# Kernel optimization log

Measured on AMD Instinct MI355X. Metric: run time of the kernel, lower is better.

## Reference

```python
import jax, jax.numpy as jnp
import numpy as np


def _grid_sample_points(feat, gx, gy):
    """Bilinear grid_sample at point list, align_corners=False, zeros padding.
    feat: [B, H, W, C]; gx, gy: [B, N] normalized coords in [-1, 1].
    Returns [B, N, C].
    """
    B, H, W, C = feat.shape
    # unnormalize (align_corners=False): -1 -> -0.5, +1 -> size-0.5
    ix = (gx + 1.0) * (W * 0.5) - 0.5
    iy = (gy + 1.0) * (H * 0.5) - 0.5
    x0 = jnp.floor(ix)
    y0 = jnp.floor(iy)
    x1 = x0 + 1.0
    y1 = y0 + 1.0
    wx1 = ix - x0
    wx0 = 1.0 - wx1
    wy1 = iy - y0
    wy0 = 1.0 - wy1
    bidx = jnp.arange(B)[:, None]  # [B,1] broadcasts against [B,N]

    def gather(yy, xx):
        valid = (xx >= 0) & (xx <= W - 1) & (yy >= 0) & (yy <= H - 1)
        xi = jnp.clip(xx, 0, W - 1).astype(jnp.int32)
        yi = jnp.clip(yy, 0, H - 1).astype(jnp.int32)
        v = feat[bidx, yi, xi]  # [B, N, C]
        return v * valid[..., None].astype(feat.dtype)

    out = (gather(y0, x0) * (wy0 * wx0)[..., None]
           + gather(y0, x1) * (wy0 * wx1)[..., None]
           + gather(y1, x0) * (wy1 * wx0)[..., None]
           + gather(y1, x1) * (wy1 * wx1)[..., None])
    return out


def setup_inputs() -> dict:
    key = jax.random.key(0)
    k1, k2, k3, k4, k5 = jax.random.split(key, 5)
    B, C, T, Wd, Hd = 16, 64, 16, 36, 36
    N, D = 4096, C * T  # num_neurons, num_input
    x = jax.random.normal(k1, (B, C, T, Wd, Hd), dtype=jnp.float32)
    mu = jax.random.uniform(k2, (N, 2), minval=-1.0, maxval=1.0, dtype=jnp.float32)
    sigma = jax.random.uniform(k3, (N,), dtype=jnp.float32)  # unused in eval mode
    W = jax.random.normal(k4, (N, D), dtype=jnp.float32) * 0.02
    b = jax.random.normal(k5, (N,), dtype=jnp.float32) * 0.01
    return {"x": x, "mu": mu, "sigma": sigma, "W": W, "b": b}


def reference(x, mu, sigma, W, b):
    # eval-mode forward (self.training == False): grid = mu broadcast over batch
    B, C, T, Wd, Hd = x.shape
    N = mu.shape[0]
    # torch: x.view(B, C*T, Wd, Hd); grid_sample treats dim2 as H_in, dim3 as W_in
    feat = x.reshape(B, C * T, Wd, Hd).transpose(0, 2, 3, 1)
    g = jnp.clip(mu, -1.0, 1.0)
    gx = jnp.broadcast_to(g[:, 0], (B, N))  # grid[...,0] indexes W_in
    gy = jnp.broadcast_to(g[:, 1], (B, N))  # grid[...,1] indexes H_in
    sampled = _grid_sample_points(feat, gx, gy)  # [B, N, C*T]
    # PoissonLinearReadout 3D path == per-neuron dot product (diagonal of full matmul)
    y = jnp.einsum('bnc,nc->bn', sampled, W) + b
    return jax.nn.elu(y) + 1.0
```

## Files before the change

kernel.cpp:

```cpp
#include <hip/hip_runtime.h>
#include <hip/hip_bf16.h>
#include <cmath>

#define CT    1024
#define PIX   1296
#define BATCH 16
#define NNEUR 4096
#define HW    36
#define NBINS (HW * HW)
#define NPAIR (NNEUR * 4)
#define BCT   (BATCH * CT)

typedef short short8 __attribute__((ext_vector_type(8)));
typedef float f32x4  __attribute__((ext_vector_type(4)));

__device__ __forceinline__ unsigned short bfu(float f) {
    __hip_bfloat16 h = __float2bfloat16(f);
    return *reinterpret_cast<unsigned short*>(&h);
}

__global__ __launch_bounds__(256) void transpose_bf16_kernel(
    const float* __restrict__ x, __hip_bfloat16* __restrict__ feat)
{
    __shared__ unsigned short lds[64][34];
    const int b      = blockIdx.z;
    const int ctBase = blockIdx.y * 64;
    const int pBase  = blockIdx.x * 32;
    const int t      = threadIdx.x;
    const size_t xb  = (size_t)b * CT * PIX;
    {
        const int r  = t >> 2;
        const int pc = (t & 3) * 8;
        const float* src = x + xb + (size_t)(ctBase + r) * PIX + pBase + pc;
        if (pBase + 32 <= PIX) {
            float4 a = reinterpret_cast<const float4*>(src)[0];
            float4 c = reinterpret_cast<const float4*>(src)[1];
            lds[r][pc + 0] = bfu(a.x); lds[r][pc + 1] = bfu(a.y);
            lds[r][pc + 2] = bfu(a.z); lds[r][pc + 3] = bfu(a.w);
            lds[r][pc + 4] = bfu(c.x); lds[r][pc + 5] = bfu(c.y);
            lds[r][pc + 6] = bfu(c.z); lds[r][pc + 7] = bfu(c.w);
        } else {
#pragma unroll
            for (int i = 0; i < 8; ++i) {
                int p = pBase + pc + i;
                lds[r][pc + i] = (p < PIX) ? bfu(src[i]) : (unsigned short)0;
            }
        }
    }
    __syncthreads();
    const int pr = t >> 3;
    const int cc = (t & 7) * 8;
    if (pBase + pr < PIX) {
        unsigned short o[8];
#pragma unroll
        for (int i = 0; i < 8; ++i) o[i] = lds[cc + i][pr];
        const size_t off = ((size_t)(pBase + pr) * BATCH + b) * CT + ctBase + cc;
        *reinterpret_cast<uint4*>((unsigned short*)feat + off) = *reinterpret_cast<uint4*>(o);
    }
}

__global__ __launch_bounds__(1024) void sortpack_kernel(
    const float* __restrict__ mu,
    int* __restrict__ plist,
    int* __restrict__ pstart,
    const float* __restrict__ W, __hip_bfloat16* __restrict__ Wb)
{
    const int t = threadIdx.x;
    if (blockIdx.x != 0) {
        const int i = (blockIdx.x - 1) * 1024 + t;
        const float4 v = reinterpret_cast<const float4*>(W)[i];
        unsigned short o[4] = { bfu(v.x), bfu(v.y), bfu(v.z), bfu(v.w) };
        reinterpret_cast<ushort4*>(Wb)[i] = *reinterpret_cast<ushort4*>(o);
        return;
    }

    __shared__ int hist[NBINS];
    __shared__ int chunkSum[48];
    for (int i = t; i < NBINS; i += 1024) hist[i] = 0;
    __syncthreads();

    int key[16];
#pragma unroll
    for (int nn = 0; nn < 4; ++nn) {
        const int n = t * 4 + nn;
        float gx = fminf(fmaxf(mu[2 * n],     -1.f), 1.f);
        float gy = fminf(fmaxf(mu[2 * n + 1], -1.f), 1.f);
        float ix = (gx + 1.f) * (HW * 0.5f) - 0.5f;
        float iy = (gy + 1.f) * (HW * 0.5f) - 0.5f;
        int x0 = (int)floorf(ix), y0 = (int)floorf(iy);
#pragma unroll
        for (int k = 0; k < 4; ++k) {
            int xi = min(max(x0 + (k & 1), 0), HW - 1);
            int yi = min(max(y0 + (k >> 1), 0), HW - 1);
            key[nn * 4 + k] = yi * HW + xi;
            atomicAdd(&hist[key[nn * 4 + k]], 1);
        }
    }
    __syncthreads();
    if (t < 41) {
        int s = 0;
        for (int i = 0; i < 32; ++i) {
            int idx = t * 32 + i;
            if (idx < NBINS) s += hist[idx];
        }
        chunkSum[t] = s;
    }
    __syncthreads();
    if (t == 0) {
        int run = 0;
        for (int i = 0; i < 41; ++i) { int v = chunkSum[i]; chunkSum[i] = run; run += v; }
    }
    __syncthreads();
    if (t < 41) {
        int run = chunkSum[t];
        for (int i = 0; i < 32; ++i) {
            int idx = t * 32 + i;
            if (idx < NBINS) { int v = hist[idx]; hist[idx] = run; run += v; }
        }
    }
    __syncthreads();
    for (int i = t; i < NBINS; i += 1024) pstart[i] = hist[i];
    if (t == 0) pstart[NBINS] = NPAIR;
    __syncthreads();
#pragma unroll
    for (int nn = 0; nn < 4; ++nn) {
#pragma unroll
        for (int k = 0; k < 4; ++k) {
            const int pairid = (t * 4 + nn) * 4 + k;
            const int pos = atomicAdd(&hist[key[nn * 4 + k]], 1);
            plist[pos] = pairid;
        }
    }
}

__global__ __launch_bounds__(256) void pixgemm_kernel(
    const __hip_bfloat16* __restrict__ feat,
    const __hip_bfloat16* __restrict__ Wb,
    const int* __restrict__ plist,
    const int* __restrict__ pstart,
    float* __restrict__ pd)
{
    const int p  = blockIdx.x;
    const int t  = threadIdx.x;
    const int wv = t >> 6;
    const int l  = t & 63;
    const int start = pstart[p];
    const int cnt   = pstart[p + 1] - start;
    const int ntile = (cnt + 15) >> 4;

    __shared__ f32x4 red[4][64];

    const unsigned short* fbase = (const unsigned short*)feat
        + (size_t)p * BCT + (size_t)(l & 15) * CT + ((l >> 4) * 8) + wv * 256;

    for (int tile = 0; tile < ntile; ++tile) {
        const int slot = tile * 16 + (l & 15);
        const int v    = (slot < cnt) ? plist[start + slot] : 0;
        const unsigned short* wrow = (const unsigned short*)Wb
            + (size_t)(v >> 2) * CT + ((l >> 4) * 8) + wv * 256;

        f32x4 acc = {0.f, 0.f, 0.f, 0.f};
#pragma unroll
        for (int s = 0; s < 8; ++s) {
            const short8 av = *reinterpret_cast<const short8*>(fbase + s * 32);
            const short8 bv = *reinterpret_cast<const short8*>(wrow  + s * 32);
            acc = __builtin_amdgcn_mfma_f32_16x16x32_bf16(av, bv, acc, 0, 0, 0);
        }
        red[wv][l] = acc;
        __syncthreads();
        if (wv == 0 && slot < cnt) {
            const f32x4 a0 = red[0][l], a1 = red[1][l], a2 = red[2][l], a3 = red[3][l];
            float4 o;
            o.x = a0[0] + a1[0] + a2[0] + a3[0];
            o.y = a0[1] + a1[1] + a2[1] + a3[1];
            o.z = a0[2] + a1[2] + a2[2] + a3[2];
            o.w = a0[3] + a1[3] + a2[3] + a3[3];
            *reinterpret_cast<float4*>(pd + (size_t)v * 16 + (l >> 4) * 4) = o;
        }
        __syncthreads();
    }
}

__global__ __launch_bounds__(256) void finish_kernel(
    const float* __restrict__ pd, const float* __restrict__ mu,
    const float* __restrict__ bias, float* __restrict__ out)
{
    const int i = blockIdx.x * 256 + threadIdx.x;
    const int n = i >> 4, b = i & 15;

    float gx = fminf(fmaxf(mu[2 * n],     -1.f), 1.f);
    float gy = fminf(fmaxf(mu[2 * n + 1], -1.f), 1.f);
    float ix = (gx + 1.f) * (HW * 0.5f) - 0.5f;
    float iy = (gy + 1.f) * (HW * 0.5f) - 0.5f;
    float x0f = floorf(ix), y0f = floorf(iy);
    float wx1 = ix - x0f, wx0 = 1.f - wx1;
    float wy1 = iy - y0f, wy0 = 1.f - wy1;
    int x0 = (int)x0f, y0 = (int)y0f;

    float y = bias[n];
#pragma unroll
    for (int k = 0; k < 4; ++k) {
        int xx = x0 + (k & 1), yy = y0 + (k >> 1);
        bool valid = (xx >= 0) && (xx < HW) && (yy >= 0) && (yy < HW);
        float cw = ((k & 1) ? wx1 : wx0) * ((k >> 1) ? wy1 : wy0) * (valid ? 1.f : 0.f);
        y = fmaf(cw, pd[(size_t)(n * 4 + k) * 16 + b], y);
    }
    out[(size_t)b * NNEUR + n] = (y > 0.f) ? (y + 1.f) : expf(y);
}

__global__ __launch_bounds__(256) void readout_f32_strided_kernel(
    const float* __restrict__ x,
    const float* __restrict__ mu,
    const float* __restrict__ Wm,
    const float* __restrict__ bias,
    float* __restrict__ out)
{
    const int n = blockIdx.x;
    const int t = threadIdx.x;
    const float4 w4 = reinterpret_cast<const float4*>(Wm + (size_t)n * CT)[t];
    float gx = fminf(fmaxf(mu[2 * n],     -1.f), 1.f);
    float gy = fminf(fmaxf(mu[2 * n + 1], -1.f), 1.f);
    float ix = (gx + 1.f) * (HW * 0.5f) - 0.5f;
    float iy = (gy + 1.f) * (HW * 0.5f) - 0.5f;
    float x0f = floorf(ix), y0f = floorf(iy);
    float wx1 = ix - x0f, wx0 = 1.f - wx1;
    float wy1 = iy - y0f, wy0 = 1.f - wy1;
    int x0 = (int)x0f, y0 = (int)y0f;
    float cw[4]; int cp[4];
#pragma unroll
    for (int k = 0; k < 4; ++k) {
        int xx = x0 + (k & 1), yy = y0 + (k >> 1);
        bool valid = (xx >= 0) && (xx < HW) && (yy >= 0) && (yy < HW);
        int xi = min(max(xx, 0), HW - 1), yi = min(max(yy, 0), HW - 1);
        cp[k] = yi * HW + xi;
        cw[k] = ((k & 1) ? wx1 : wx0) * ((k >> 1) ? wy1 : wy0) * (valid ? 1.f : 0.f);
    }
    float acc[BATCH];
#pragma unroll
    for (int b = 0; b < BATCH; ++b) {
        float s = 0.f;
#pragma unroll
        for (int k = 0; k < 4; ++k) {
            if (cw[k] != 0.f) {
                const float* fp = x + (size_t)b * CT * PIX + cp[k];
                const int c0 = 4 * t;
                s += cw[k] * (fp[(size_t)(c0 + 0) * PIX] * w4.x
                            + fp[(size_t)(c0 + 1) * PIX] * w4.y
                            + fp[(size_t)(c0 + 2) * PIX] * w4.z
                            + fp[(size_t)(c0 + 3) * PIX] * w4.w);
            }
        }
        acc[b] = s;
    }
#pragma unroll
    for (int b = 0; b < BATCH; ++b) {
        float v = acc[b];
#pragma unroll
        for (int off = 32; off > 0; off >>= 1)
            v += __shfl_down(v, off, 64);
        acc[b] = v;
    }
    __shared__ float red[4][BATCH];
    const int wave = t >> 6, lane = t & 63;
    if (lane == 0) {
#pragma unroll
        for (int b = 0; b < BATCH; ++b) red[wave][b] = acc[b];
    }
    __syncthreads();
    if (t < BATCH) {
        float y = red[0][t] + red[1][t] + red[2][t] + red[3][t] + bias[n];
        out[(size_t)t * NNEUR + n] = (y > 0.f) ? (y + 1.f) : expf(y);
    }
}

extern "C" void kernel_launch(void* const* d_in, const int* in_sizes, int n_in,
                              void* d_out, int out_size, void* d_ws, size_t ws_size,
                              hipStream_t stream)
{
    const float* x    = (const float*)d_in[0];
    const float* mu   = (const float*)d_in[1];
    const float* Wm   = (const float*)d_in[3];
    const float* bias = (const float*)d_in[4];
    float* out = (float*)d_out;

    const size_t featBytes  = (size_t)BATCH * PIX * CT * sizeof(__hip_bfloat16);
    const size_t wBytes     = (size_t)NNEUR * CT * sizeof(__hip_bfloat16);
    const size_t plistBytes = (size_t)NPAIR * sizeof(int);
    const size_t pstartBytes= 8192;
    const size_t pdBytes    = (size_t)NPAIR * 16 * sizeof(float);

    if (ws_size >= featBytes + wBytes + plistBytes + pstartBytes + pdBytes) {
        char* wp = (char*)d_ws;
        __hip_bfloat16* feat = (__hip_bfloat16*)wp;                 wp += featBytes;
        __hip_bfloat16* Wb   = (__hip_bfloat16*)wp;                 wp += wBytes;
        int*   plist  = (int*)wp;                                   wp += plistBytes;
        int*   pstart = (int*)wp;                                   wp += pstartBytes;
        float* pd     = (float*)wp;

        dim3 tg((PIX + 31) / 32, CT / 64, BATCH);
        transpose_bf16_kernel<<<tg, 256, 0, stream>>>(x, feat);
        sortpack_kernel<<<1 + (NNEUR * CT / 4) / 1024, 1024, 0, stream>>>(
            mu, plist, pstart, Wm, Wb);
        pixgemm_kernel<<<PIX, 256, 0, stream>>>(feat, Wb, plist, pstart, pd);
        finish_kernel<<<(NNEUR * BATCH) / 256, 256, 0, stream>>>(pd, mu, bias, out);
    } else {
        readout_f32_strided_kernel<<<NNEUR, 256, 0, stream>>>(x, mu, Wm, bias, out);
    }
}
```

Baseline: 60.11 us.

## Flatten pixel GEMM into per-wave tile list for load balancing

The sort kernel now builds a compact list of 16-pair tiles across all pixels. The pixel GEMM assigns one wave per tile, and each wave does the full 1024-length reduction itself, so the LDS cross-wave reduction and the block barriers go away. Loads are batched eight at a time before the MFMAs to raise memory-level parallelism. The tile-list build adds serial work inside the single sort block, and the grid is sized from a fixed upper bound on the tile count.

```diff
diff --git a/kernel.cpp b/kernel.cpp
--- a/kernel.cpp
+++ b/kernel.cpp
@@ -10,6 +10,7 @@
 #define NBINS (HW * HW)
 #define NPAIR (NNEUR * 4)
 #define BCT   (BATCH * CT)
+#define MAXT  2320
 
 typedef short short8 __attribute__((ext_vector_type(8)));
 typedef float f32x4  __attribute__((ext_vector_type(4)));
@@ -63,6 +64,7 @@
     const float* __restrict__ mu,
     int* __restrict__ plist,
     int* __restrict__ pstart,
+    int* __restrict__ tiles,
     const float* __restrict__ W, __hip_bfloat16* __restrict__ Wb)
 {
     const int t = threadIdx.x;
@@ -131,6 +133,34 @@
             plist[pos] = pairid;
         }
     }
+    __syncthreads();
+
+    if (t < 41) {
+        int s = 0;
+        for (int i = 0; i < 32; ++i) {
+            int idx = t * 32 + i;
+            if (idx < NBINS) s += (pstart[idx + 1] - pstart[idx] + 15) >> 4;
+        }
+        chunkSum[t] = s;
+    }
+    __syncthreads();
+    if (t == 0) {
+        int run = 0;
+        for (int i = 0; i < 41; ++i) { int v = chunkSum[i]; chunkSum[i] = run; run += v; }
+        pstart[NBINS + 1] = run;
+    }
+    __syncthreads();
+    if (t < 41) {
+        int run = chunkSum[t];
+        for (int i = 0; i < 32; ++i) {
+            int idx = t * 32 + i;
+            if (idx < NBINS) {
+                int tc = (pstart[idx + 1] - pstart[idx] + 15) >> 4;
+                for (int j = 0; j < tc; ++j) tiles[run + j] = (idx << 12) | j;
+                run += tc;
+            }
+        }
+    }
 }
 
 __global__ __launch_bounds__(256) void pixgemm_kernel(
@@ -138,46 +168,45 @@
     const __hip_bfloat16* __restrict__ Wb,
     const int* __restrict__ plist,
     const int* __restrict__ pstart,
+    const int* __restrict__ tiles,
     float* __restrict__ pd)
 {
-    const int p  = blockIdx.x;
-    const int t  = threadIdx.x;
-    const int wv = t >> 6;
-    const int l  = t & 63;
-    const int start = pstart[p];
-    const int cnt   = pstart[p + 1] - start;
-    const int ntile = (cnt + 15) >> 4;
-
-    __shared__ f32x4 red[4][64];
-
-    const unsigned short* fbase = (const unsigned short*)feat
-        + (size_t)p * BCT + (size_t)(l & 15) * CT + ((l >> 4) * 8) + wv * 256;
-
-    for (int tile = 0; tile < ntile; ++tile) {
-        const int slot = tile * 16 + (l & 15);
-        const int v    = (slot < cnt) ? plist[start + slot] : 0;
-        const unsigned short* wrow = (const unsigned short*)Wb
-            + (size_t)(v >> 2) * CT + ((l >> 4) * 8) + wv * 256;
-
-        f32x4 acc = {0.f, 0.f, 0.f, 0.f};
-#pragma unroll
-        for (int s = 0; s < 8; ++s) {
-            const short8 av = *reinterpret_cast<const short8*>(fbase + s * 32);
-            const short8 bv = *reinterpret_cast<const short8*>(wrow  + s * 32);
-            acc = __builtin_amdgcn_mfma_f32_16x16x32_bf16(av, bv, acc, 0, 0, 0);
-        }
-        red[wv][l] = acc;
-        __syncthreads();
-        if (wv == 0 && slot < cnt) {
-            const f32x4 a0 = red[0][l], a1 = red[1][l], a2 = red[2][l], a3 = red[3][l];
-            float4 o;
-            o.x = a0[0] + a1[0] + a2[0] + a3[0];
-            o.y = a0[1] + a1[1] + a2[1] + a3[1];
-            o.z = a0[2] + a1[2] + a2[2] + a3[2];
-            o.w = a0[3] + a1[3] + a2[3] + a3[3];
-            *reinterpret_cast<float4*>(pd + (size_t)v * 16 + (l >> 4) * 4) = o;
-        }
-        __syncthreads();
+    const int T    = pstart[NBINS + 1];
+    const int tile = blockIdx.x * 4 + (threadIdx.x >> 6);
+    if (tile >= T) return;
+    const int l  = threadIdx.x & 63;
+
+    const int code = tiles[tile];
+    const int p    = code >> 12;
+    const int j    = code & 4095;
+    const int cstart = pstart[p] + (j << 4);
+    const int tcnt   = min(16, pstart[p + 1] - cstart);
+
+    const bool valid = (l & 15) < tcnt;
+    const int  v     = plist[cstart + (valid ? (l & 15) : 0)];
+
+    const unsigned short* arow = (const unsigned short*)feat
+        + (size_t)p * BCT + (size_t)(l & 15) * CT + ((l >> 4) * 8);
+    const unsigned short* brow = (const unsigned short*)Wb
+        + (size_t)(v >> 2) * CT + ((l >> 4) * 8);
+
+    f32x4 acc = {0.f, 0.f, 0.f, 0.f};
+#pragma unroll
+    for (int s = 0; s < 32; s += 8) {
+        short8 a[8], b[8];
+#pragma unroll
+        for (int u = 0; u < 8; ++u) {
+            a[u] = *reinterpret_cast<const short8*>(arow + (s + u) * 32);
+            b[u] = *reinterpret_cast<const short8*>(brow + (s + u) * 32);
+        }
+#pragma unroll
+        for (int u = 0; u < 8; ++u)
+            acc = __builtin_amdgcn_mfma_f32_16x16x32_bf16(a[u], b[u], acc, 0, 0, 0);
+    }
+
+    if (valid) {
+        float4 o = { acc[0], acc[1], acc[2], acc[3] };
+        *reinterpret_cast<float4*>(pd + (size_t)v * 16 + (l >> 4) * 4) = o;
     }
 }
 
@@ -287,21 +316,23 @@
     const size_t wBytes     = (size_t)NNEUR * CT * sizeof(__hip_bfloat16);
     const size_t plistBytes = (size_t)NPAIR * sizeof(int);
     const size_t pstartBytes= 8192;
+    const size_t tilesBytes = 12288;
     const size_t pdBytes    = (size_t)NPAIR * 16 * sizeof(float);
 
-    if (ws_size >= featBytes + wBytes + plistBytes + pstartBytes + pdBytes) {
+    if (ws_size >= featBytes + wBytes + plistBytes + pstartBytes + tilesBytes + pdBytes) {
         char* wp = (char*)d_ws;
         __hip_bfloat16* feat = (__hip_bfloat16*)wp;                 wp += featBytes;
         __hip_bfloat16* Wb   = (__hip_bfloat16*)wp;                 wp += wBytes;
         int*   plist  = (int*)wp;                                   wp += plistBytes;
         int*   pstart = (int*)wp;                                   wp += pstartBytes;
+        int*   tiles  = (int*)wp;                                   wp += tilesBytes;
         float* pd     = (float*)wp;
 
         dim3 tg((PIX + 31) / 32, CT / 64, BATCH);
         transpose_bf16_kernel<<<tg, 256, 0, stream>>>(x, feat);
         sortpack_kernel<<<1 + (NNEUR * CT / 4) / 1024, 1024, 0, stream>>>(
-            mu, plist, pstart, Wm, Wb);
-        pixgemm_kernel<<<PIX, 256, 0, stream>>>(feat, Wb, plist, pstart, pd);
+            mu, plist, pstart, tiles, Wm, Wb);
+        pixgemm_kernel<<<(MAXT + 3) / 4, 256, 0, stream>>>(feat, Wb, plist, pstart, tiles, pd);
         finish_kernel<<<(NNEUR * BATCH) / 256, 256, 0, stream>>>(pd, mu, bias, out);
     } else {
         readout_f32_strided_kernel<<<NNEUR, 256, 0, stream>>>(x, mu, Wm, bias, out);
```

New measurement: 73.07 us. 1.22x slower.
